# Kernel optimization log

Hardware: AMD Instinct MI355X
Metric: run time of the kernel (lower is better)

## Reference

```python
import jax, jax.numpy as jnp
import numpy as np

L = 4096
EMBED = 512
KEY = 512
VAL = 512
HEADS = 8

def _linear_params(key, fan_in, fan_out):
    k1, k2 = jax.random.split(key)
    w = jax.random.normal(k1, (fan_in, fan_out), jnp.float32) * 0.02
    b = jax.random.normal(k2, (fan_out,), jnp.float32) * 0.02
    return w, b

def setup_inputs() -> dict:
    key = jax.random.key(0)
    ks = jax.random.split(key, 9)
    x = jax.random.normal(ks[0], (L, EMBED), jnp.float32)
    shortest_path = jax.random.normal(ks[1], (L, L), jnp.float32)
    wq_w, wq_b = _linear_params(ks[2], EMBED, KEY)
    wk_w, wk_b = _linear_params(ks[3], EMBED, KEY)
    wv_w, wv_b = _linear_params(ks[4], EMBED, VAL)
    qp_w, qp_b = _linear_params(ks[5], KEY, KEY)
    kp_w, kp_b = _linear_params(ks[6], KEY, KEY)
    vp_w, vp_b = _linear_params(ks[7], VAL, VAL)
    out_w, out_b = _linear_params(ks[8], VAL, EMBED)
    return dict(x=x, shortest_path=shortest_path,
                wq_w=wq_w, wq_b=wq_b, wk_w=wk_w, wk_b=wk_b, wv_w=wv_w, wv_b=wv_b,
                qp_w=qp_w, qp_b=qp_b, kp_w=kp_w, kp_b=kp_b, vp_w=vp_w, vp_b=vp_b,
                out_w=out_w, out_b=out_b)

def reference(x, shortest_path, wq_w, wq_b, wk_w, wk_b, wv_w, wv_b,
              qp_w, qp_b, kp_w, kp_b, vp_w, vp_b, out_w, out_b):
    H = HEADS
    dh = KEY // H   # q/k head dim
    dv = VAL // H   # v head dim
    # two-stage projections
    q = (x @ wq_w + wq_b) @ qp_w + qp_b          # [L, KEY]
    k = (x @ wk_w + wk_b) @ kp_w + kp_b          # [L, KEY]
    v = (x @ wv_w + wv_b) @ vp_w + vp_b          # [L, VAL]
    q = q.reshape(L, H, dh).transpose(1, 0, 2)   # [H, L, dh]
    k = k.reshape(L, H, dh).transpose(1, 0, 2)
    v = v.reshape(L, H, dv).transpose(1, 0, 2)   # [H, L, dv]
    att = jnp.einsum('hqd,hkd->hqk', q, k) / jnp.sqrt(jnp.float32(dh))  # [H, L, L]
    sp = jax.nn.softmax(shortest_path, axis=-1) * 0.5                   # [L, L]
    att = jax.nn.softmax(att + sp[None, :, :], axis=-1)                 # [H, L, L]
    out = jnp.einsum('hqk,hkd->hqd', att, v)     # [H, L, dv]
    out = out.transpose(1, 0, 2).reshape(L, VAL)
    return out @ out_w + out_b                   # [L, EMBED]
```

## Files before the change

kernel.cpp:

```cpp
#include <hip/hip_runtime.h>

typedef _Float16 f16;
typedef __fp16 fp16x2 __attribute__((ext_vector_type(2)));
typedef _Float16 f16x4 __attribute__((ext_vector_type(4)));
typedef _Float16 f16x8 __attribute__((ext_vector_type(8)));
typedef float f32x4 __attribute__((ext_vector_type(4)));
typedef float f32x16 __attribute__((ext_vector_type(16)));

#define L_SEQ 4096
#define D_MODEL 512
#define KVSPLIT 4

__device__ __forceinline__ void gload16(const void* g, void* l) {
  __builtin_amdgcn_global_load_lds((const __attribute__((address_space(1))) void*)g,
                                   (__attribute__((address_space(3))) void*)l, 16, 0, 0);
}

__global__ void cvt4_kernel(const float* __restrict__ s0, const float* __restrict__ s1,
                            const float* __restrict__ s2, const float* __restrict__ s3,
                            f16* __restrict__ d0, f16* __restrict__ d1,
                            f16* __restrict__ d2, f16* __restrict__ d3) {
  const float* s; f16* d; int n4;
  switch (blockIdx.z) {
    case 0: s = s0; d = d0; n4 = 524288; break;
    case 1: s = s1; d = d1; n4 = 65536; break;
    case 2: s = s2; d = d2; n4 = 65536; break;
    default: s = s3; d = d3; n4 = 65536; break;
  }
  for (int i = blockIdx.x * 256 + threadIdx.x; i < n4; i += 131072) {
    float4 v = ((const float4*)s)[i];
    f16x4 o;
    o[0] = (f16)v.x; o[1] = (f16)v.y; o[2] = (f16)v.z; o[3] = (f16)v.w;
    ((f16x4*)d)[i] = o;
  }
}

__global__ void transpose4_kernel(
    const float* __restrict__ s0, const float* __restrict__ s1,
    const float* __restrict__ s2, const float* __restrict__ s3,
    f16* __restrict__ d0, f16* __restrict__ d1, f16* __restrict__ d2, f16* __restrict__ d3)
{
  const float* s; f16* d;
  switch (blockIdx.z) {
    case 0: s = s0; d = d0; break;
    case 1: s = s1; d = d1; break;
    case 2: s = s2; d = d2; break;
    default: s = s3; d = d3; break;
  }
  __shared__ float tl[32][33];
  const int bx = blockIdx.x * 32, by = blockIdx.y * 32;
  const int tx = threadIdx.x, ty = threadIdx.y;
  #pragma unroll
  for (int i = 0; i < 4; ++i)
    tl[ty + i * 8][tx] = s[(size_t)(by + ty + i * 8) * 512 + bx + tx];
  __syncthreads();
  #pragma unroll
  for (int i = 0; i < 4; ++i)
    d[(size_t)(bx + ty + i * 8) * 512 + by + tx] = (f16)tl[tx][ty + i * 8];
}

template<int MODE, int BM>
__device__ __forceinline__ void gemm_core(
    const f16* __restrict__ A, const f16* __restrict__ BT,
    const float* __restrict__ bias, void* __restrict__ Cv,
    int M, int N, int K, f16* As, f16* Bs)
{
  constexpr int MI = BM / 32;
  const int t = threadIdx.x;
  const int w = t >> 6;
  const int bm = blockIdx.x * BM, bn = blockIdx.y * 64;
  const int m0 = (w >> 1) * (BM / 2), n0 = (w & 1) * 32;
  const int lane = t & 63, lr = lane & 15, lg = lane >> 4;

  f32x4 zf = {0.f, 0.f, 0.f, 0.f};
  f32x4 acc[MI][2];
  #pragma unroll
  for (int i = 0; i < MI; ++i)
    #pragma unroll
    for (int j = 0; j < 2; ++j)
      acc[i][j] = zf;

  const int arow = t >> 2, achk = t & 3;
  const f16* gA = A + (size_t)(bm + arow) * K + achk * 8;
  const f16* gB = BT + (size_t)(bn + arow) * K + achk * 8;
  f16* lA = As + w * 512;
  f16* lB = Bs + w * 512;

  for (int k0 = 0; k0 < K; k0 += 32) {
    gload16(gA + k0, lA);
    if constexpr (BM == 128) gload16(gA + (size_t)64 * K + k0, lA + 2048);
    gload16(gB + k0, lB);
    __syncthreads();
    f16x8 af[MI], bfv[2];
    #pragma unroll
    for (int i = 0; i < MI; ++i)
      af[i] = *(const f16x8*)&As[(m0 + i * 16 + lr) * 32 + lg * 8];
    #pragma unroll
    for (int j = 0; j < 2; ++j)
      bfv[j] = *(const f16x8*)&Bs[(n0 + j * 16 + lr) * 32 + lg * 8];
    #pragma unroll
    for (int i = 0; i < MI; ++i)
      #pragma unroll
      for (int j = 0; j < 2; ++j)
        acc[i][j] = __builtin_amdgcn_mfma_f32_16x16x32_f16(af[i], bfv[j], acc[i][j], 0, 0, 0);
    __syncthreads();
  }

  #pragma unroll
  for (int j = 0; j < 2; ++j) {
    const int gn = bn + n0 + j * 16 + lr;
    const float bv = (MODE == 3) ? 0.f : bias[gn];
    #pragma unroll
    for (int i = 0; i < MI; ++i) {
      const int gmb = bm + m0 + i * 16 + lg * 4;
      if constexpr (MODE == 0 || MODE == 3) {
        f16* C = (f16*)Cv;
        #pragma unroll
        for (int r = 0; r < 4; ++r)
          C[(size_t)(gmb + r) * N + gn] = (f16)(acc[i][j][r] + bv);
      } else if constexpr (MODE == 1) {
        f16* C = (f16*)Cv;
        f16x4 u;
        u[0] = (f16)(acc[i][j][0] + bv);
        u[1] = (f16)(acc[i][j][1] + bv);
        u[2] = (f16)(acc[i][j][2] + bv);
        u[3] = (f16)(acc[i][j][3] + bv);
        *(f16x4*)&C[(size_t)gn * M + gmb] = u;
      } else {
        float* C = (float*)Cv;
        #pragma unroll
        for (int r = 0; r < 4; ++r)
          C[(size_t)(gmb + r) * N + gn] = acc[i][j][r] + bv;
      }
    }
  }
}

template<int MODE, int BM>
__global__ __launch_bounds__(256) void gemm_bt_kernel(
    const f16* __restrict__ A, const f16* __restrict__ BT,
    const float* __restrict__ bias, void* __restrict__ Cv, int M, int N, int K)
{
  __shared__ __attribute__((aligned(16))) f16 As[BM * 32];
  __shared__ __attribute__((aligned(16))) f16 Bs[64 * 32];
  gemm_core<MODE, BM>(A, BT, bias, Cv, M, N, K, As, Bs);
}

__global__ __launch_bounds__(256) void wcombine_kernel(
    const f16* __restrict__ qpT, const f16* __restrict__ kpT, const f16* __restrict__ vpT,
    const f16* __restrict__ wq16, const f16* __restrict__ wk16, const f16* __restrict__ wv16,
    f16* __restrict__ WqT, f16* __restrict__ WkT, f16* __restrict__ WvT)
{
  __shared__ __attribute__((aligned(16))) f16 As[128 * 32];
  __shared__ __attribute__((aligned(16))) f16 Bs[64 * 32];
  const f16* A; const f16* B; f16* C;
  switch (blockIdx.z) {
    case 0: A = qpT; B = wq16; C = WqT; break;
    case 1: A = kpT; B = wk16; C = WkT; break;
    default: A = vpT; B = wv16; C = WvT; break;
  }
  gemm_core<3, 128>(A, B, nullptr, C, 512, 512, 512, As, Bs);
}

__global__ void bcombine_kernel(
    const float* __restrict__ wq_b, const float* __restrict__ wk_b, const float* __restrict__ wv_b,
    const f16* __restrict__ qpT, const f16* __restrict__ kpT, const f16* __restrict__ vpT,
    const float* __restrict__ qp_b, const float* __restrict__ kp_b, const float* __restrict__ vp_b,
    float* __restrict__ bc)
{
  const float* b1; const f16* WT; const float* b2;
  switch (blockIdx.z) {
    case 0: b1 = wq_b; WT = qpT; b2 = qp_b; break;
    case 1: b1 = wk_b; WT = kpT; b2 = kp_b; break;
    default: b1 = wv_b; WT = vpT; b2 = vp_b; break;
  }
  const int o = blockIdx.x * 256 + threadIdx.x;
  const f16* row = WT + (size_t)o * 512;
  float s = 0.f;
  #pragma unroll 8
  for (int m = 0; m < 512; ++m)
    s += b1[m] * (float)row[m];
  bc[blockIdx.z * 512 + o] = s + b2[o];
}

__global__ __launch_bounds__(256) void gemm_qkv_kernel(
    const f16* __restrict__ x,
    const f16* __restrict__ WqT, const f16* __restrict__ WkT, const f16* __restrict__ WvT,
    const float* __restrict__ bc,
    f16* __restrict__ q_f, f16* __restrict__ k_f, f16* __restrict__ vT)
{
  __shared__ __attribute__((aligned(16))) f16 As[128 * 32];
  __shared__ __attribute__((aligned(16))) f16 Bs[64 * 32];
  const int z = blockIdx.z;
  if (z == 2)
    gemm_core<1, 128>(x, WvT, bc + 1024, vT, 4096, 512, 512, As, Bs);
  else if (z == 1)
    gemm_core<0, 128>(x, WkT, bc + 512, k_f, 4096, 512, 512, As, Bs);
  else
    gemm_core<0, 128>(x, WqT, bc, q_f, 4096, 512, 512, As, Bs);
}

__global__ __launch_bounds__(512) void sp_bias_kernel(
    const float* __restrict__ spg, f16* __restrict__ bt)
{
  __shared__ __attribute__((aligned(16))) f16 ex[16 * 4104];
  __shared__ float sums[16];
  const int t = threadIdx.x;

  {
    const int row = t >> 5, j = t & 31;
    const float4* srow = (const float4*)(spg + (size_t)(blockIdx.x * 16 + row) * L_SEQ);
    f16* dst = ex + row * 4104;
    float ssum = 0.f;
    #pragma unroll 4
    for (int c = 0; c < 32; ++c) {
      float4 v = srow[c * 32 + j];
      float e0 = __expf(v.x), e1 = __expf(v.y), e2 = __expf(v.z), e3 = __expf(v.w);
      ssum += (e0 + e1) + (e2 + e3);
      f16x4 u;
      u[0] = (f16)e0; u[1] = (f16)e1; u[2] = (f16)e2; u[3] = (f16)e3;
      *(f16x4*)&dst[(c * 32 + j) * 4] = u;
    }
    ssum += __shfl_xor(ssum, 1, 64);
    ssum += __shfl_xor(ssum, 2, 64);
    ssum += __shfl_xor(ssum, 4, 64);
    ssum += __shfl_xor(ssum, 8, 64);
    ssum += __shfl_xor(ssum, 16, 64);
    if (j == 0) sums[row] = ssum;
  }
  __syncthreads();

  const int hi = t & 1, qloc = (t >> 1) & 15, s16 = (t >> 5) & 1;
  const float sc = 0.5f / sums[qloc];
  const int qt5 = blockIdx.x >> 1;
  const int q31 = ((blockIdx.x & 1) << 4) + qloc;
  const f16* exr = ex + qloc * 4104 + s16 * 16 + hi * 8;
  f16* ob = bt + (size_t)qt5 * 131072 + s16 * 512 + q31 * 16 + hi * 8;
  #pragma unroll 4
  for (int i = 0; i < 16; ++i) {
    const int kt5 = (t >> 6) + i * 8;
    f16x8 v = *(const f16x8*)&exr[kt5 * 32];
    f16x8 u;
    #pragma unroll
    for (int e = 0; e < 8; ++e)
      u[e] = (f16)__log2f(fmaf((float)v[e], sc, 1.0f));
    *(f16x8*)&ob[(size_t)kt5 * 1024] = u;
  }
}

__global__ __launch_bounds__(256, 4) void attn3_kernel(
    const f16* __restrict__ qg, const f16* __restrict__ kg,
    const f16* __restrict__ vTg, const f16* __restrict__ bt,
    f16* __restrict__ opart, float* __restrict__ rspart)
{
  __shared__ __attribute__((aligned(16))) f16 Ks[2 * 4096];
  __shared__ __attribute__((aligned(16))) f16 Vs[2 * 4096];

  const int t = threadIdx.x;
  const int w = t >> 6, lane = t & 63;
  const int l31 = lane & 31, hi = lane >> 5;
  const int b = blockIdx.x;
  const int h = (b >> 3) & 7;
  const int g = (b & 7) + ((b >> 6) << 3);
  const int qt = g & 31;
  const int z = g >> 5;
  const int q0w = qt * 128 + w * 32;
  const int kvbase = z * (L_SEQ / KVSPLIT);
  const int NST = (L_SEQ / KVSPLIT) / 64;

  f16x8 qf[4];
  #pragma unroll
  for (int dk = 0; dk < 4; ++dk)
    qf[dk] = *(const f16x8*)&qg[(size_t)(q0w + l31) * D_MODEL + h * 64 + dk * 16 + hi * 8];

  const int srow0 = t >> 3, srow1 = 32 + (t >> 3), q16 = t & 7;
  const f16* ksrc0 = kg + h * 64 + (size_t)(kvbase + srow0) * D_MODEL + ((q16 ^ (srow0 & 7)) * 8);
  const f16* ksrc1 = kg + h * 64 + (size_t)(kvbase + srow1) * D_MODEL + ((q16 ^ (srow1 & 7)) * 8);
  const f16* vsrc0 = vTg + (size_t)(h * 64 + srow0) * L_SEQ + kvbase + (q16 ^ (srow0 & 7)) * 8;
  const f16* vsrc1 = vTg + (size_t)(h * 64 + srow1) * L_SEQ + kvbase + (q16 ^ (srow1 & 7)) * 8;

  #define STAGE(buf, stp)                                                      \
    do {                                                                       \
      const size_t ko = (size_t)(stp) * 64 * D_MODEL, vo = (size_t)(stp) * 64; \
      gload16(ksrc0 + ko, &Ks[(buf) * 4096 + w * 512]);                        \
      gload16(ksrc1 + ko, &Ks[(buf) * 4096 + 2048 + w * 512]);                 \
      gload16(vsrc0 + vo, &Vs[(buf) * 4096 + w * 512]);                        \
      gload16(vsrc1 + vo, &Vs[(buf) * 4096 + 2048 + w * 512]);                 \
    } while (0)

  const int sw23 = (l31 & ~12) | ((l31 & 4) << 1) | ((l31 & 8) >> 1);
  const int r7 = sw23 & 7;
  const int krow0 = sw23 * 64, krow1 = krow0 + 2048;
  const int vr7 = l31 & 7;
  const int vrow0 = l31 * 64, vrow1 = vrow0 + 2048;

  const f16* bb = bt + (size_t)(q0w >> 5) * 131072 + l31 * 16 + hi * 8;
  const int kvb5 = kvbase >> 5;

  f32x16 zz = {0,0,0,0,0,0,0,0,0,0,0,0,0,0,0,0};
  f32x16 o0 = zz, o1 = zz;
  float rs = 0.f;

  STAGE(0, 0);
  __syncthreads();

  for (int st = 0; st < NST; ++st) {
    const int buf = st & 1;
    if (st + 1 < NST) STAGE(buf ^ 1, st + 1);

    const f16* bs = bb + (size_t)(kvb5 + st * 2) * 1024;
    f16x8 bl[4];
    bl[0] = *(const f16x8*)(bs);
    bl[1] = *(const f16x8*)(bs + 512);
    bl[2] = *(const f16x8*)(bs + 1024);
    bl[3] = *(const f16x8*)(bs + 1536);

    f32x16 s0 = zz, s1 = zz;
    const f16* kb = &Ks[buf * 4096];
    #pragma unroll
    for (int dk = 0; dk < 4; ++dk) {
      const int ch = ((dk * 2 + hi) ^ r7) * 8;
      f16x8 k0 = *(const f16x8*)&kb[krow0 + ch];
      f16x8 k1 = *(const f16x8*)&kb[krow1 + ch];
      s0 = __builtin_amdgcn_mfma_f32_32x32x16_f16(k0, qf[dk], s0, 0, 0, 0);
      s1 = __builtin_amdgcn_mfma_f32_32x32x16_f16(k1, qf[dk], s1, 0, 0, 0);
    }

    f16x8 pa[4];
    #pragma unroll
    for (int jj = 0; jj < 2; ++jj) {
      const f32x16& s = jj ? s1 : s0;
      float pv[16];
      #pragma unroll
      for (int r = 0; r < 16; ++r) {
        const float lb = (float)bl[jj * 2 + (r >> 3)][r & 7];
        pv[r] = __builtin_amdgcn_exp2f(fmaf(s[r], 0.18033688f, lb));
      }
      #pragma unroll
      for (int sh = 0; sh < 2; ++sh) {
        union { fp16x2 h2[4]; f16x8 v; } u;
        u.h2[0] = __builtin_amdgcn_cvt_pkrtz(pv[sh * 8 + 0], pv[sh * 8 + 1]);
        u.h2[1] = __builtin_amdgcn_cvt_pkrtz(pv[sh * 8 + 2], pv[sh * 8 + 3]);
        u.h2[2] = __builtin_amdgcn_cvt_pkrtz(pv[sh * 8 + 4], pv[sh * 8 + 5]);
        u.h2[3] = __builtin_amdgcn_cvt_pkrtz(pv[sh * 8 + 6], pv[sh * 8 + 7]);
        pa[jj * 2 + sh] = u.v;
      }
    }

#if __has_builtin(__builtin_amdgcn_fdot2)
    {
      const fp16x2 one2 = {(__fp16)1.0f, (__fp16)1.0f};
      #pragma unroll
      for (int kk = 0; kk < 4; ++kk) {
        const fp16x2* hp = (const fp16x2*)&pa[kk];
        #pragma unroll
        for (int e = 0; e < 4; ++e)
          rs = __builtin_amdgcn_fdot2(hp[e], one2, rs, false);
      }
    }
#else
    #pragma unroll
    for (int kk = 0; kk < 4; ++kk)
      #pragma unroll
      for (int e = 0; e < 8; ++e)
        rs += (float)pa[kk][e];
#endif

    const f16* vb = &Vs[buf * 4096];
    #pragma unroll
    for (int kk = 0; kk < 4; ++kk) {
      const int ch = ((kk * 2 + hi) ^ vr7) * 8;
      f16x8 v0 = *(const f16x8*)&vb[vrow0 + ch];
      f16x8 v1 = *(const f16x8*)&vb[vrow1 + ch];
      o0 = __builtin_amdgcn_mfma_f32_32x32x16_f16(pa[kk], v0, o0, 0, 0, 0);
      o1 = __builtin_amdgcn_mfma_f32_32x32x16_f16(pa[kk], v1, o1, 0, 0, 0);
    }
    __syncthreads();
  }
  #undef STAGE

  rs += __shfl_xor(rs, 32, 64);
  f16* op = opart + (size_t)z * (L_SEQ * D_MODEL);
  #pragma unroll
  for (int dg = 0; dg < 2; ++dg) {
    const f32x16& o = dg ? o1 : o0;
    #pragma unroll
    for (int r = 0; r < 16; ++r) {
      const int q = q0w + (r & 3) + 8 * (r >> 2) + 4 * hi;
      op[(size_t)q * D_MODEL + h * 64 + dg * 32 + l31] = (f16)o[r];
    }
  }
  if (hi == 0)
    rspart[((size_t)z * 8 + h) * L_SEQ + q0w + l31] = rs;
}

__global__ void combine4_kernel(const f16* __restrict__ opart,
                                const float* __restrict__ rspart,
                                f16* __restrict__ attout)
{
  const int idx = blockIdx.x * 256 + threadIdx.x;
  const int q = idx >> 6;
  const int d = (idx & 63) << 3;
  const int h = d >> 6;
  float rsum = 0.f;
  #pragma unroll
  for (int zz = 0; zz < KVSPLIT; ++zz)
    rsum += rspart[((size_t)zz * 8 + h) * L_SEQ + q];
  const float inv = 1.f / rsum;
  float acc[8] = {0,0,0,0,0,0,0,0};
  #pragma unroll
  for (int zz = 0; zz < KVSPLIT; ++zz) {
    f16x8 v = *(const f16x8*)&opart[(size_t)zz * (L_SEQ * D_MODEL) + (size_t)q * D_MODEL + d];
    #pragma unroll
    for (int e = 0; e < 8; ++e) acc[e] += (float)v[e];
  }
  f16x8 u;
  #pragma unroll
  for (int e = 0; e < 8; ++e) u[e] = (f16)(acc[e] * inv);
  *(f16x8*)&attout[(size_t)q * D_MODEL + d] = u;
}

extern "C" void kernel_launch(void* const* d_in, const int* in_sizes, int n_in,
                              void* d_out, int out_size, void* d_ws, size_t ws_size,
                              hipStream_t stream)
{
  (void)in_sizes; (void)n_in; (void)out_size; (void)ws_size;

  const float* x    = (const float*)d_in[0];
  const float* sp   = (const float*)d_in[1];
  const float* wq_w = (const float*)d_in[2];
  const float* wq_b = (const float*)d_in[3];
  const float* wk_w = (const float*)d_in[4];
  const float* wk_b = (const float*)d_in[5];
  const float* wv_w = (const float*)d_in[6];
  const float* wv_b = (const float*)d_in[7];
  const float* qp_w = (const float*)d_in[8];
  const float* qp_b = (const float*)d_in[9];
  const float* kp_w = (const float*)d_in[10];
  const float* kp_b = (const float*)d_in[11];
  const float* vp_w = (const float*)d_in[12];
  const float* vp_b = (const float*)d_in[13];
  const float* out_w = (const float*)d_in[14];
  const float* out_b = (const float*)d_in[15];

  const size_t MB = 1048576;
  char* ws = (char*)d_ws;
  f16*   x_f    = (f16*)(ws + 0);
  f16*   qpT    = (f16*)(ws + 4 * MB);
  f16*   kpT    = (f16*)(ws + 4 * MB + 524288);
  f16*   vpT    = (f16*)(ws + 5 * MB);
  f16*   wq16   = (f16*)(ws + 6 * MB);
  f16*   wk16   = (f16*)(ws + 6 * MB + 524288);
  f16*   wv16   = (f16*)(ws + 7 * MB);
  f16*   WqT    = (f16*)(ws + 7 * MB + 524288);
  f16*   WkT    = (f16*)(ws + 8 * MB);
  f16*   WvT    = (f16*)(ws + 8 * MB + 524288);
  float* bc     = (float*)(ws + 9 * MB);
  f16*   opart  = (f16*)(ws + 0);
  f16*   q_f    = (f16*)(ws + 16 * MB);
  f16*   attout = (f16*)(ws + 16 * MB);
  f16*   k_f    = (f16*)(ws + 20 * MB);
  f16*   vT     = (f16*)(ws + 24 * MB);
  float* rspart = (float*)(ws + 28 * MB);
  f16*   bt     = (f16*)(ws + 28 * MB + 524288);
  f16*   outT   = (f16*)(ws + 60 * MB + 524288);

  cvt4_kernel<<<dim3(512, 1, 4), 256, 0, stream>>>(x, wq_w, wk_w, wv_w,
                                                   x_f, wq16, wk16, wv16);
  transpose4_kernel<<<dim3(16, 16, 4), dim3(32, 8), 0, stream>>>(
      qp_w, kp_w, vp_w, out_w, qpT, kpT, vpT, outT);
  sp_bias_kernel<<<256, 512, 0, stream>>>(sp, bt);

  wcombine_kernel<<<dim3(4, 8, 3), 256, 0, stream>>>(qpT, kpT, vpT,
                                                     wq16, wk16, wv16,
                                                     WqT, WkT, WvT);
  bcombine_kernel<<<dim3(2, 1, 3), 256, 0, stream>>>(wq_b, wk_b, wv_b,
                                                     qpT, kpT, vpT,
                                                     qp_b, kp_b, vp_b, bc);
  gemm_qkv_kernel<<<dim3(32, 8, 3), 256, 0, stream>>>(x_f, WqT, WkT, WvT, bc,
                                                      q_f, k_f, vT);

  attn3_kernel<<<dim3(1024), 256, 0, stream>>>(q_f, k_f, vT, bt,
                                               opart, rspart);
  combine4_kernel<<<1024, 256, 0, stream>>>(opart, rspart, attout);

  gemm_bt_kernel<2, 64><<<dim3(64, 8), 256, 0, stream>>>(attout, outT, out_b,
                                                         d_out, 4096, 512, 512);
}
```

Baseline: 132.9 us.

## Fine-grained vmcnt waits for KV prefetch and compute row sums via MFMA

Replaces __syncthreads around the double-buffered K/V staging with explicit s_waitcnt vmcnt counts and raw s_barrier. The next stage's loads are issued after the bias loads and only the current buffer's loads are waited on, which is meant to overlap global-to-LDS transfer with compute. The softmax row-sum is no longer built from fdot2 VALU reductions but from an extra MFMA against a ones vector. This adds a third MFMA per step and relies on exact vmcnt counting (bias loads counted too) for correctness.

```diff
diff --git a/kernel.cpp b/kernel.cpp
--- a/kernel.cpp
+++ b/kernel.cpp
@@ -298,15 +298,14 @@
   const int kvb5 = kvbase >> 5;
 
   f32x16 zz = {0,0,0,0,0,0,0,0,0,0,0,0,0,0,0,0};
-  f32x16 o0 = zz, o1 = zz;
-  float rs = 0.f;
+  f32x16 o0 = zz, o1 = zz, ors = zz;
+  const f16x8 ones = {(f16)1.f, (f16)1.f, (f16)1.f, (f16)1.f,
+                      (f16)1.f, (f16)1.f, (f16)1.f, (f16)1.f};
 
   STAGE(0, 0);
-  __syncthreads();
 
   for (int st = 0; st < NST; ++st) {
     const int buf = st & 1;
-    if (st + 1 < NST) STAGE(buf ^ 1, st + 1);
 
     const f16* bs = bb + (size_t)(kvb5 + st * 2) * 1024;
     f16x8 bl[4];
@@ -314,6 +313,16 @@
     bl[1] = *(const f16x8*)(bs + 512);
     bl[2] = *(const f16x8*)(bs + 1024);
     bl[3] = *(const f16x8*)(bs + 1536);
+    __builtin_amdgcn_sched_barrier(0);
+
+    if (st + 1 < NST) {
+      STAGE(buf ^ 1, st + 1);
+      asm volatile("s_waitcnt vmcnt(8)" ::: "memory");
+    } else {
+      asm volatile("s_waitcnt vmcnt(4)" ::: "memory");
+    }
+    __builtin_amdgcn_s_barrier();
+    __builtin_amdgcn_sched_barrier(0);
 
     f32x16 s0 = zz, s1 = zz;
     const f16* kb = &Ks[buf * 4096];
@@ -347,25 +356,6 @@
       }
     }
 
-#if __has_builtin(__builtin_amdgcn_fdot2)
-    {
-      const fp16x2 one2 = {(__fp16)1.0f, (__fp16)1.0f};
-      #pragma unroll
-      for (int kk = 0; kk < 4; ++kk) {
-        const fp16x2* hp = (const fp16x2*)&pa[kk];
-        #pragma unroll
-        for (int e = 0; e < 4; ++e)
-          rs = __builtin_amdgcn_fdot2(hp[e], one2, rs, false);
-      }
-    }
-#else
-    #pragma unroll
-    for (int kk = 0; kk < 4; ++kk)
-      #pragma unroll
-      for (int e = 0; e < 8; ++e)
-        rs += (float)pa[kk][e];
-#endif
-
     const f16* vb = &Vs[buf * 4096];
     #pragma unroll
     for (int kk = 0; kk < 4; ++kk) {
@@ -374,12 +364,14 @@
       f16x8 v1 = *(const f16x8*)&vb[vrow1 + ch];
       o0 = __builtin_amdgcn_mfma_f32_32x32x16_f16(pa[kk], v0, o0, 0, 0, 0);
       o1 = __builtin_amdgcn_mfma_f32_32x32x16_f16(pa[kk], v1, o1, 0, 0, 0);
-    }
-    __syncthreads();
+      ors = __builtin_amdgcn_mfma_f32_32x32x16_f16(pa[kk], ones, ors, 0, 0, 0);
+    }
+
+    __builtin_amdgcn_sched_barrier(0);
+    __builtin_amdgcn_s_barrier();
   }
   #undef STAGE
 
-  rs += __shfl_xor(rs, 32, 64);
   f16* op = opart + (size_t)z * (L_SEQ * D_MODEL);
   #pragma unroll
   for (int dg = 0; dg < 2; ++dg) {
@@ -390,8 +382,11 @@
       op[(size_t)q * D_MODEL + h * 64 + dg * 32 + l31] = (f16)o[r];
     }
   }
-  if (hi == 0)
-    rspart[((size_t)z * 8 + h) * L_SEQ + q0w + l31] = rs;
+  if (l31 == 0) {
+    #pragma unroll
+    for (int r = 0; r < 16; ++r)
+      rspart[((size_t)z * 8 + h) * L_SEQ + q0w + (r & 3) + 8 * (r >> 2) + 4 * hi] = ors[r];
+  }
 }
 
 __global__ void combine4_kernel(const f16* __restrict__ opart,
```

Result: slower. 168.8 us (+27.0%).
